# Kernel tuning notes

Hardware: AMD Instinct MI355X
Metric: run time of the kernel (lower is better)

The kernel has to match this reference:

```python
import math
import jax, jax.numpy as jnp
import numpy as np

NEG_INF = -1e9


def maximum_path(neg_cent, text_len, spec_len):
    """Monotonic alignment search (VITS). neg_cent: [B, Ty(spec), Tx(text)].
    Returns hard path [B, Ty, Tx] (float32, 0/1)."""
    B, Ty, Tx = neg_cent.shape
    xs = jnp.arange(Tx)

    # Forward DP over spec frames y; carry = best cumulative value per text pos x.
    def fwd_step(value, inp):
        y, score = inp  # score: [B, Tx]
        diag = jnp.pad(value[:, :-1], ((0, 0), (1, 0)), constant_values=NEG_INF)
        d = diag > value  # move-diagonally indicator for backtracking
        new = score + jnp.maximum(value, diag)
        new = jnp.where(y == 0, jnp.where(xs == 0, score, NEG_INF), new)
        return new, d

    init = jnp.full((B, Tx), NEG_INF, dtype=neg_cent.dtype)
    _, dirs = jax.lax.scan(fwd_step, init,
                           (jnp.arange(Ty), jnp.swapaxes(neg_cent, 0, 1)))
    # dirs: [Ty, B, Tx] bool; dirs[y] compares row y-1 values (as in cython MAS).

    # Backtrack from (spec_len-1, text_len-1) down to y=0.
    def bwd_step(index, inp):
        y, d_row = inp  # index: [B] int32, d_row: [B, Tx]
        active = y < spec_len  # [B]
        row = jnp.where(active[:, None],
                        jax.nn.one_hot(index, Tx, dtype=jnp.float32), 0.0)
        d_at = jnp.take_along_axis(d_row, index[:, None], axis=1)[:, 0]
        move = (index != 0) & ((index == y) | d_at)
        index = jnp.where(active & move, index - 1, index)
        return index, row

    init_idx = text_len - 1
    _, path = jax.lax.scan(bwd_step, init_idx, (jnp.arange(Ty), dirs),
                           reverse=True)
    return jnp.swapaxes(path, 0, 1)  # [B, Ty, Tx]


def setup_inputs() -> dict:
    key = jax.random.key(0)
    ks = jax.random.split(key, 6)
    B, C, Tx, Ty = 8, 192, 512, 2048
    z_p = jax.random.normal(ks[0], (B, C, Ty), dtype=jnp.float32)
    m_p = jax.random.normal(ks[1], (B, C, Tx), dtype=jnp.float32)
    logs_p = 0.1 * jax.random.normal(ks[2], (B, C, Tx), dtype=jnp.float32)
    logs_q = 0.1 * jax.random.normal(ks[3], (B, C, Ty), dtype=jnp.float32)
    text_len = jax.random.randint(ks[4], (B,), Tx * 3 // 4, Tx + 1)
    spec_len = jax.random.randint(ks[5], (B,), Ty * 3 // 4, Ty + 1)
    text_mask = (jnp.arange(Tx)[None, :] < text_len[:, None]).astype(jnp.float32)[:, None, :]
    spec_mask = (jnp.arange(Ty)[None, :] < spec_len[:, None]).astype(jnp.float32)[:, None, :]
    return {"z_p": z_p, "m_p": m_p, "logs_p": logs_p, "logs_q": logs_q,
            "text_mask": text_mask, "spec_mask": spec_mask}


def reference(z_p, m_p, logs_p, logs_q, text_mask, spec_mask):
    text_len = jnp.sum(text_mask, axis=(1, 2)).astype(jnp.int32)  # [B]
    spec_len = jnp.sum(spec_mask, axis=(1, 2)).astype(jnp.int32)  # [B]

    # ---- search_path: neg log-likelihood grid [B, T_spec, T_text] ----
    s_p_sq_r = jnp.exp(-2.0 * logs_p)  # [B, C, Tx]
    nc1 = jnp.sum(-0.5 * math.log(2 * math.pi) - logs_p, axis=1, keepdims=True)  # [B,1,Tx]
    nc2 = jnp.einsum('bct,bcx->btx', -0.5 * z_p * z_p, s_p_sq_r)
    nc3 = jnp.einsum('bct,bcx->btx', z_p, m_p * s_p_sq_r)
    nc4 = jnp.sum(-0.5 * m_p * m_p * s_p_sq_r, axis=1, keepdims=True)  # [B,1,Tx]
    neg_cent = nc1 + nc2 + nc3 + nc4  # [B, Ty, Tx]

    MAS_path = maximum_path(neg_cent, text_len, spec_len)  # [B, Ty, Tx]

    # ---- gather-combine text stats onto spec frames ----
    m_p_a = jnp.einsum('btx,bcx->bct', MAS_path, m_p)      # [B, C, Ty]
    logs_p_a = jnp.einsum('btx,bcx->bct', MAS_path, logs_p)

    # ---- KL divergence loss (VITS) ----
    kl = logs_p_a - logs_q - 0.5 \
        + 0.5 * jnp.square(z_p - m_p_a) * jnp.exp(-2.0 * logs_p_a)
    loss_kl = jnp.sum(kl * spec_mask) / jnp.sum(spec_mask)

    duration = jnp.sum(MAS_path, axis=1)[:, None, :]  # [B, 1, Tx]
    return MAS_path[:, None], m_p_a, logs_p_a, loss_kl, duration
```

## Files before the change

### kernel.cpp

```cpp
#include <hip/hip_runtime.h>
#include <cstdint>
#include <cstddef>

#define BB 8
#define CC 192
#define TXX 512
#define TYY 2048

#define NEG_INF (-1e9f)
#define HALF_LOG_2PI 0.9189385332046727f

#define O1 8388608
#define O2 11534336
#define O3 14680064
#define O4 14680065

#define WS_NEG   0
#define WS_S     33554432
#define WS_MSR   36700160
#define WS_BIAS  39845888
#define WS_DIRS  39862272
#define WS_IDX   40910848
#define WS_LENS  40976384
#define WS_PART  40976448

typedef float f32x4 __attribute__((ext_vector_type(4)));

#define PRE_NZERO 2048
#define PRE_NPREP 3072
#define PRE_NBIAS 16
#define PRE_NLEN  8
__global__ __launch_bounds__(256) void k_pre(const float* __restrict__ logs_p,
                                             const float* __restrict__ m_p,
                                             const float* __restrict__ tmask,
                                             const float* __restrict__ smask,
                                             float* __restrict__ s,
                                             float* __restrict__ msr,
                                             float* __restrict__ bias,
                                             int* __restrict__ lens,
                                             float* __restrict__ out) {
    int blk = blockIdx.x, tid = threadIdx.x;
    if (blk < PRE_NZERO) {
        int64_t i = (int64_t)blk * 256 + tid;
        const int64_t n4 = (int64_t)BB * TYY * TXX / 4;
        float4 z4 = make_float4(0.f, 0.f, 0.f, 0.f);
        float4* p4 = (float4*)out;
        for (int64_t k = i; k < n4; k += (int64_t)PRE_NZERO * 256) p4[k] = z4;
        if (i < BB * TXX) out[O4 + i] = 0.0f;
    } else if (blk < PRE_NZERO + PRE_NPREP) {
        int i = (blk - PRE_NZERO) * 256 + tid;
        float lp = logs_p[i], m = m_p[i];
        float sv = expf(-2.0f * lp);
        s[i] = sv;
        msr[i] = m * sv;
    } else if (blk < PRE_NZERO + PRE_NPREP + PRE_NBIAS) {
        int i = (blk - PRE_NZERO - PRE_NPREP) * 256 + tid;
        int b = i >> 9, x = i & (TXX - 1);
        size_t base = (size_t)b * CC * TXX + x;
        const float* lpb = logs_p + base;
        const float* mb  = m_p + base;
        float acc = 0.f;
#pragma unroll 8
        for (int c = 0; c < CC; ++c) {
            float lp = lpb[(size_t)c * TXX];
            float m  = mb[(size_t)c * TXX];
            float msv = m * expf(-2.0f * lp);
            acc += -HALF_LOG_2PI - lp - 0.5f * m * msv;
        }
        bias[i] = acc;
    } else {
        __shared__ float red[256];
        int b = blk - (PRE_NZERO + PRE_NPREP + PRE_NBIAS);
        float ts = 0.f;
        for (int i = tid; i < TXX; i += 256) ts += tmask[b * TXX + i];
        red[tid] = ts; __syncthreads();
        for (int s2 = 128; s2 > 0; s2 >>= 1) { if (tid < s2) red[tid] += red[tid + s2]; __syncthreads(); }
        if (tid == 0) lens[b] = (int)(red[0] + 0.5f);
        __syncthreads();
        float ss = 0.f;
        for (int i = tid; i < TYY; i += 256) ss += smask[b * TYY + i];
        red[tid] = ss; __syncthreads();
        for (int s2 = 128; s2 > 0; s2 >>= 1) { if (tid < s2) red[tid] += red[tid + s2]; __syncthreads(); }
        if (tid == 0) lens[8 + b] = (int)(red[0] + 0.5f);
    }
}

__global__ __launch_bounds__(256) void k_gemm(const float* __restrict__ z,
                                              const float* __restrict__ msr,
                                              const float* __restrict__ sarr,
                                              const float* __restrict__ bias,
                                              const int* __restrict__ lens,
                                              float* __restrict__ neg) {
    int x0 = blockIdx.x * 64, t0 = blockIdx.y * 64, b = blockIdx.z;
    if (x0 >= lens[b] || t0 >= lens[8 + b]) return;

    __shared__ float Zs[16][68], Ms[16][68], Ss[16][68];
    int tid = threadIdx.x;
    int tx = tid & 15, ty = tid >> 4;
    const float* zb = z    + (size_t)b * CC * TYY;
    const float* mb = msr  + (size_t)b * CC * TXX;
    const float* sb = sarr + (size_t)b * CC * TXX;
    int lr = tid >> 4, lc = (tid & 15) * 4;
    float acc[4][4] = {};
    for (int k0 = 0; k0 < CC; k0 += 16) {
        float4 zv = *(const float4*)(zb + (size_t)(k0 + lr) * TYY + t0 + lc);
        float4 mv = *(const float4*)(mb + (size_t)(k0 + lr) * TXX + x0 + lc);
        float4 sv = *(const float4*)(sb + (size_t)(k0 + lr) * TXX + x0 + lc);
        __syncthreads();
        *(float4*)&Zs[lr][lc] = zv;
        *(float4*)&Ms[lr][lc] = mv;
        *(float4*)&Ss[lr][lc] = sv;
        __syncthreads();
#pragma unroll
        for (int k = 0; k < 16; ++k) {
            float4 a4  = *(const float4*)&Zs[k][ty * 4];
            float4 bm4 = *(const float4*)&Ms[k][tx * 4];
            float4 bs4 = *(const float4*)&Ss[k][tx * 4];
            float av[4]  = {a4.x, a4.y, a4.z, a4.w};
            float bmv[4] = {bm4.x, bm4.y, bm4.z, bm4.w};
            float bsv[4] = {bs4.x, bs4.y, bs4.z, bs4.w};
#pragma unroll
            for (int i2 = 0; i2 < 4; ++i2) {
                float a2 = -0.5f * av[i2] * av[i2];
#pragma unroll
                for (int j = 0; j < 4; ++j)
                    acc[i2][j] += av[i2] * bmv[j] + a2 * bsv[j];
            }
        }
    }
    float4 b4 = *(const float4*)(bias + b * TXX + x0 + tx * 4);
    float bv[4] = {b4.x, b4.y, b4.z, b4.w};
#pragma unroll
    for (int i2 = 0; i2 < 4; ++i2) {
        int t = t0 + ty * 4 + i2;
        float4 o;
        o.x = acc[i2][0] + bv[0]; o.y = acc[i2][1] + bv[1];
        o.z = acc[i2][2] + bv[2]; o.w = acc[i2][3] + bv[3];
        *(float4*)(neg + ((size_t)b * TYY + t) * TXX + x0 + tx * 4) = o;
    }
}

#define GLOAD4(DST, PTR, OFF)                                             \
    asm volatile("global_load_dwordx4 %0, %1, off offset:" #OFF           \
                 : "=v"(DST) : "v"(PTR) : "memory")

#define WAIT_VM(N) do {                                                   \
    asm volatile("s_waitcnt vmcnt(" #N ")" ::: "memory");                 \
    __builtin_amdgcn_sched_barrier(0);                                    \
} while (0)

#define LOADG(DST, G) do {                                                \
    const char* p0_ = (const char*)nc4 + (size_t)(G) * 16384 + lane * 32; \
    const char* p2_ = p0_ + 4096;                                         \
    const char* p4_ = p0_ + 8192;                                         \
    const char* p6_ = p0_ + 12288;                                        \
    GLOAD4(DST[0],  p0_, 0);    GLOAD4(DST[1],  p0_, 16);                 \
    GLOAD4(DST[2],  p0_, 2048); GLOAD4(DST[3],  p0_, 2064);               \
    GLOAD4(DST[4],  p2_, 0);    GLOAD4(DST[5],  p2_, 16);                 \
    GLOAD4(DST[6],  p2_, 2048); GLOAD4(DST[7],  p2_, 2064);               \
    GLOAD4(DST[8],  p4_, 0);    GLOAD4(DST[9],  p4_, 16);                 \
    GLOAD4(DST[10], p4_, 2048); GLOAD4(DST[11], p4_, 2064);               \
    GLOAD4(DST[12], p6_, 0);    GLOAD4(DST[13], p6_, 16);                 \
    GLOAD4(DST[14], p6_, 2048); GLOAD4(DST[15], p6_, 2064);               \
} while (0)

#define DPROW(CUR, YB, R) do {                                                \
    int y_ = (YB) + (R);                                                      \
    float s0_ = CUR[2*(R)][0],   s1_ = CUR[2*(R)][1];                         \
    float s2_ = CUR[2*(R)][2],   s3_ = CUR[2*(R)][3];                         \
    float s4_ = CUR[2*(R)+1][0], s5_ = CUR[2*(R)+1][1];                       \
    float s6_ = CUR[2*(R)+1][2], s7_ = CUR[2*(R)+1][3];                       \
    unsigned d_ = 0;                                                          \
    if (y_ == 0) {                                                            \
        if (lane == 0) v[0] = s0_;             \
    } else {                                                                  \
        float pl_ = __int_as_float(__builtin_amdgcn_update_dpp(               \
            0, __float_as_int(v[7]), 0x138, 0xF, 0xF, false));                \
        if (lane == 0) pl_ = NEG_INF;                                         \
        float n0_ = s0_ + fmaxf(v[0], pl_);  if (pl_  > v[0]) d_ |= 1u;       \
        float n1_ = s1_ + fmaxf(v[1], v[0]); if (v[0] > v[1]) d_ |= 2u;       \
        float n2_ = s2_ + fmaxf(v[2], v[1]); if (v[1] > v[2]) d_ |= 4u;       \
        float n3_ = s3_ + fmaxf(v[3], v[2]); if (v[2] > v[3]) d_ |= 8u;       \
        float n4_ = s4_ + fmaxf(v[4], v[3]); if (v[3] > v[4]) d_ |= 16u;      \
        float n5_ = s5_ + fmaxf(v[5], v[4]); if (v[4] > v[5]) d_ |= 32u;      \
        float n6_ = s6_ + fmaxf(v[6], v[5]); if (v[5] > v[6]) d_ |= 64u;      \
        float n7_ = s7_ + fmaxf(v[7], v[6]); if (v[6] > v[7]) d_ |= 128u;     \
        v[0] = n0_; v[1] = n1_; v[2] = n2_; v[3] = n3_;                       \
        v[4] = n4_; v[5] = n5_; v[6] = n6_; v[7] = n7_;                       \
    }                                                                         \
    unsigned t_ = (unsigned)(y_ - 8 * lane);                                  \
    if (t_ < 8u) d_ |= 1u << t_;                 \
    acc |= d_ << (((R) & 3) * 8);                                             \
    if (((R) & 3) == 3) { db32[(y_ >> 2) * 64 + lane] = acc; acc = 0; }       \
} while (0)

#define FWD_ITER(G, CUR, NXT) do {                                \
    int g_ = (G);                                                 \
    if (g_ + 2 < ng) {                                            \
        LOADG(NXT, g_ + 2);                 \
        WAIT_VM(32);                                              \
    } else if (g_ + 1 < ng) {                                     \
        WAIT_VM(16);                                              \
    } else {                                                      \
        WAIT_VM(0);                                               \
    }                                                             \
    int yb_ = 8 * g_;                                             \
    DPROW(CUR, yb_, 0); DPROW(CUR, yb_, 1);                       \
    DPROW(CUR, yb_, 2); DPROW(CUR, yb_, 3);                       \
    DPROW(CUR, yb_, 4); DPROW(CUR, yb_, 5);                       \
    DPROW(CUR, yb_, 6); DPROW(CUR, yb_, 7);                       \
} while (0)

__global__ __launch_bounds__(64, 1) void k_fwd(const float* __restrict__ neg,
                                               const int* __restrict__ lens,
                                               uint32_t* __restrict__ dirs) {
    int b = blockIdx.x, lane = threadIdx.x;
    const float* nc4 = neg + (size_t)b * TYY * TXX;
    uint32_t* db32 = dirs + (size_t)b * (TYY / 4) * 64;
    int slen = lens[8 + b];
    int ng = (slen + 7) >> 3;

    float v[8];
#pragma unroll
    for (int j = 0; j < 8; ++j) v[j] = NEG_INF;
    unsigned acc = 0;

    f32x4 bufA[16], bufB[16], bufC[16];
    LOADG(bufA, 0);
    LOADG(bufB, 1);

    for (int p = 0; p < ng; p += 3) {
        FWD_ITER(p, bufA, bufC);
        if (p + 1 < ng) FWD_ITER(p + 1, bufB, bufA);
        if (p + 2 < ng) FWD_ITER(p + 2, bufC, bufB);
    }
}

#define LOADW(D0, D1, D2, WB, QROW, BOFF) do {                            \
    const uint32_t* p_ = db32 + (QROW) + 4 * (WB);                        \
    uint32_t a0_=p_[0], a1_=p_[1], a2_=p_[2],  a3_=p_[3];                 \
    uint32_t b0_=p_[4], b1_=p_[5], b2_=p_[6],  b3_=p_[7];                 \
    uint32_t c0_=p_[8], c1_=p_[9], c2_=p_[10], c3_=p_[11];                \
    D0 = ((a0_>>(BOFF))&0xffu)        | (((a1_>>(BOFF))&0xffu)<<8) |      \
         (((a2_>>(BOFF))&0xffu)<<16)  | (((a3_>>(BOFF))&0xffu)<<24);      \
    D1 = ((b0_>>(BOFF))&0xffu)        | (((b1_>>(BOFF))&0xffu)<<8) |      \
         (((b2_>>(BOFF))&0xffu)<<16)  | (((b3_>>(BOFF))&0xffu)<<24);      \
    D2 = ((c0_>>(BOFF))&0xffu)        | (((c1_>>(BOFF))&0xffu)<<8) |      \
         (((c2_>>(BOFF))&0xffu)<<16)  | (((c3_>>(BOFF))&0xffu)<<24);      \
} while (0)

__global__ __launch_bounds__(64, 1) void k_bwd(const int* __restrict__ lens,
                                               const uint32_t* __restrict__ dirs,
                                               int* __restrict__ idx_map,
                                               float* __restrict__ out) {
    int b = blockIdx.x, lane = threadIdx.x;
    const uint32_t* db32 = dirs + (size_t)b * (TYY / 4) * 64;
    int tlen = lens[b], slen = lens[8 + b];

    int idx = tlen - 1;
    int y0 = slen - 1;
    int wb;
    uint32_t W0 = 0, W1 = 0, W2 = 0;
    {
        int yy = y0 - lane; if (yy < 0) yy = 0;
        int qrow = (yy >> 2) * 64, boff = (yy & 3) * 8;
        int t = (idx >> 5) - 1; if (t < 0) t = 0; if (t > 13) t = 13;
        wb = t;
        if (lane < 32) LOADW(W0, W1, W2, wb, qrow, boff);
    }
    while (y0 >= 0) {
        int w0 = (idx >> 5) - 1; if (w0 < 0) w0 = 0; if (w0 > 14) w0 = 14;
        int s = w0 - wb; if (s < 0) s = 0; if (s > 1) s = 1;
        uint32_t lo = s ? W1 : W0;
        uint32_t hi = s ? W2 : W1;
        int base = (wb + s) << 5;
        uint32_t N0 = 0, N1 = 0, N2 = 0;
        int idxm = idx - 32; if (idxm < 0) idxm = 0;
        int wbn = (idxm >> 5) - 1; if (wbn < 0) wbn = 0; if (wbn > 13) wbn = 13;
        {
            int yn = y0 - 32 - lane; if (yn < 0) yn = 0;
            int qn = (yn >> 2) * 64, bn = (yn & 3) * 8;
            if (lane < 32) LOADW(N0, N1, N2, wbn, qn, bn);
        }
        int nsteps = (y0 + 1 < 32) ? y0 + 1 : 32;
        int cap = 0;
#pragma unroll
        for (int j = 0; j < 32; ++j) {
            if (lane == j) cap = idx;
            uint32_t l = (uint32_t)__builtin_amdgcn_readlane((int)lo, j);
            uint32_t h = (uint32_t)__builtin_amdgcn_readlane((int)hi, j);
            int bp = idx - base;
            uint32_t word = (bp & 32) ? h : l;
            idx -= (int)((word >> (bp & 31)) & 1u);
        }
        if (lane < nsteps) {
            int y = y0 - lane;
            idx_map[b * TYY + y] = cap;
            out[((size_t)(b * TYY + y)) * TXX + cap] = 1.0f;
            atomicAdd(&out[O4 + b * TXX + cap], 1.0f);
        }
        wb = wbn; W0 = N0; W1 = N1; W2 = N2;
        y0 -= 32;
    }
}

__global__ __launch_bounds__(256) void k_gather(const float* __restrict__ z_p,
                                                const float* __restrict__ m_p,
                                                const float* __restrict__ logs_p,
                                                const float* __restrict__ logs_q,
                                                const int* __restrict__ lens,
                                                const int* __restrict__ idx_map,
                                                float* __restrict__ out,
                                                float* __restrict__ partials) {
    const int S = BB * CC * TYY / 4;
    int base = blockIdx.x * 256 + threadIdx.x;
    float klsum = 0.f;
#pragma unroll
    for (int r = 0; r < 4; ++r) {
        int i = base + r * S;
        int t = i & (TYY - 1);
        int bc = i >> 11;
        int b = bc / CC;
        float ma = 0.f, la = 0.f;
        if (t < lens[8 + b]) {
            int x = idx_map[b * TYY + t];
            size_t off = (size_t)bc * TXX + x;
            ma = m_p[off];
            la = logs_p[off];
            float zv = z_p[i], lq = logs_q[i];
            float dz = zv - ma;
            klsum += la - lq - 0.5f + 0.5f * dz * dz * expf(-2.0f * la);
        }
        out[O1 + i] = ma;
        out[O2 + i] = la;
    }
    for (int o = 32; o > 0; o >>= 1) klsum += __shfl_down(klsum, o);
    __shared__ float red[4];
    if ((threadIdx.x & 63) == 0) red[threadIdx.x >> 6] = klsum;
    __syncthreads();
    if (threadIdx.x == 0) partials[blockIdx.x] = red[0] + red[1] + red[2] + red[3];
}

__global__ void k_final(const float* __restrict__ partials, const int* __restrict__ lens,
                        float* __restrict__ out) {
    float s = 0.f;
    for (int i = threadIdx.x; i < 3072; i += 256) s += partials[i];
    for (int o = 32; o > 0; o >>= 1) s += __shfl_down(s, o);
    __shared__ float red[4];
    if ((threadIdx.x & 63) == 0) red[threadIdx.x >> 6] = s;
    __syncthreads();
    if (threadIdx.x == 0) {
        float tot = 0.f;
        for (int b = 0; b < 8; ++b) tot += (float)lens[8 + b];
        out[O3] = (red[0] + red[1] + red[2] + red[3]) / tot;
    }
}

extern "C" void kernel_launch(void* const* d_in, const int* in_sizes, int n_in,
                              void* d_out, int out_size, void* d_ws, size_t ws_size,
                              hipStream_t stream) {
    const float* z_p    = (const float*)d_in[0];
    const float* m_p    = (const float*)d_in[1];
    const float* logs_p = (const float*)d_in[2];
    const float* logs_q = (const float*)d_in[3];
    const float* tmask  = (const float*)d_in[4];
    const float* smask  = (const float*)d_in[5];
    float* out = (float*)d_out;
    char* ws = (char*)d_ws;

    float*    neg      = (float*)(ws + WS_NEG);
    float*    sarr     = (float*)(ws + WS_S);
    float*    msr      = (float*)(ws + WS_MSR);
    float*    bias     = (float*)(ws + WS_BIAS);
    uint32_t* dirs     = (uint32_t*)(ws + WS_DIRS);
    int*      idx_map  = (int*)(ws + WS_IDX);
    int*      lens     = (int*)(ws + WS_LENS);
    float*    partials = (float*)(ws + WS_PART);

    hipLaunchKernelGGL(k_pre, dim3(PRE_NZERO + PRE_NPREP + PRE_NBIAS + PRE_NLEN),
                       dim3(256), 0, stream,
                       logs_p, m_p, tmask, smask, sarr, msr, bias, lens, out);
    hipLaunchKernelGGL(k_gemm,   dim3(8, 32, 8), dim3(256), 0, stream,
                       z_p, msr, sarr, bias, lens, neg);
    hipLaunchKernelGGL(k_fwd,    dim3(8),        dim3(64),  0, stream, neg, lens, dirs);
    hipLaunchKernelGGL(k_bwd,    dim3(8),        dim3(64),  0, stream, lens, dirs, idx_map, out);
    hipLaunchKernelGGL(k_gather, dim3(3072),     dim3(256), 0, stream,
                       z_p, m_p, logs_p, logs_q, lens, idx_map, out, partials);
    hipLaunchKernelGGL(k_final,  dim3(1),        dim3(256), 0, stream, partials, lens, out);
}
```

Baseline: 525.4 us.

## Fuse GEMM, forward DP and backtrack into one kernel with per-chunk flag sync

Merges the neg_cent GEMM, the forward DP scan and the backtrack into a single kernel. The first 8 blocks run the per-batch DP and spin on per-(batch, 64-row chunk) atomic counters, which GEMM tile blocks increment with release semantics when their tile is written. The forward scan can therefore start on early rows while later GEMM tiles are still being computed, and two launch boundaries disappear. The risks are spin-wait overhead, DP blocks occupying CUs, and a possible deadlock if the DP blocks run before the GEMM blocks can be scheduled. The counters reuse the partials workspace region and are zeroed by an extra block in k_pre.

```diff
diff --git a/kernel.cpp b/kernel.cpp
--- a/kernel.cpp
+++ b/kernel.cpp
@@ -38,7 +38,8 @@
                                              float* __restrict__ msr,
                                              float* __restrict__ bias,
                                              int* __restrict__ lens,
-                                             float* __restrict__ out) {
+                                             float* __restrict__ out,
+                                             int* __restrict__ cnt) {
     int blk = blockIdx.x, tid = threadIdx.x;
     if (blk < PRE_NZERO) {
         int64_t i = (int64_t)blk * 256 + tid;
@@ -68,7 +69,7 @@
             acc += -HALF_LOG_2PI - lp - 0.5f * m * msv;
         }
         bias[i] = acc;
-    } else {
+    } else if (blk < PRE_NZERO + PRE_NPREP + PRE_NBIAS + PRE_NLEN) {
         __shared__ float red[256];
         int b = blk - (PRE_NZERO + PRE_NPREP + PRE_NBIAS);
         float ts = 0.f;
@@ -82,61 +83,8 @@
         red[tid] = ss; __syncthreads();
         for (int s2 = 128; s2 > 0; s2 >>= 1) { if (tid < s2) red[tid] += red[tid + s2]; __syncthreads(); }
         if (tid == 0) lens[8 + b] = (int)(red[0] + 0.5f);
-    }
-}
-
-__global__ __launch_bounds__(256) void k_gemm(const float* __restrict__ z,
-                                              const float* __restrict__ msr,
-                                              const float* __restrict__ sarr,
-                                              const float* __restrict__ bias,
-                                              const int* __restrict__ lens,
-                                              float* __restrict__ neg) {
-    int x0 = blockIdx.x * 64, t0 = blockIdx.y * 64, b = blockIdx.z;
-    if (x0 >= lens[b] || t0 >= lens[8 + b]) return;
-
-    __shared__ float Zs[16][68], Ms[16][68], Ss[16][68];
-    int tid = threadIdx.x;
-    int tx = tid & 15, ty = tid >> 4;
-    const float* zb = z    + (size_t)b * CC * TYY;
-    const float* mb = msr  + (size_t)b * CC * TXX;
-    const float* sb = sarr + (size_t)b * CC * TXX;
-    int lr = tid >> 4, lc = (tid & 15) * 4;
-    float acc[4][4] = {};
-    for (int k0 = 0; k0 < CC; k0 += 16) {
-        float4 zv = *(const float4*)(zb + (size_t)(k0 + lr) * TYY + t0 + lc);
-        float4 mv = *(const float4*)(mb + (size_t)(k0 + lr) * TXX + x0 + lc);
-        float4 sv = *(const float4*)(sb + (size_t)(k0 + lr) * TXX + x0 + lc);
-        __syncthreads();
-        *(float4*)&Zs[lr][lc] = zv;
-        *(float4*)&Ms[lr][lc] = mv;
-        *(float4*)&Ss[lr][lc] = sv;
-        __syncthreads();
-#pragma unroll
-        for (int k = 0; k < 16; ++k) {
-            float4 a4  = *(const float4*)&Zs[k][ty * 4];
-            float4 bm4 = *(const float4*)&Ms[k][tx * 4];
-            float4 bs4 = *(const float4*)&Ss[k][tx * 4];
-            float av[4]  = {a4.x, a4.y, a4.z, a4.w};
-            float bmv[4] = {bm4.x, bm4.y, bm4.z, bm4.w};
-            float bsv[4] = {bs4.x, bs4.y, bs4.z, bs4.w};
-#pragma unroll
-            for (int i2 = 0; i2 < 4; ++i2) {
-                float a2 = -0.5f * av[i2] * av[i2];
-#pragma unroll
-                for (int j = 0; j < 4; ++j)
-                    acc[i2][j] += av[i2] * bmv[j] + a2 * bsv[j];
-            }
-        }
-    }
-    float4 b4 = *(const float4*)(bias + b * TXX + x0 + tx * 4);
-    float bv[4] = {b4.x, b4.y, b4.z, b4.w};
-#pragma unroll
-    for (int i2 = 0; i2 < 4; ++i2) {
-        int t = t0 + ty * 4 + i2;
-        float4 o;
-        o.x = acc[i2][0] + bv[0]; o.y = acc[i2][1] + bv[1];
-        o.z = acc[i2][2] + bv[2]; o.w = acc[i2][3] + bv[3];
-        *(float4*)(neg + ((size_t)b * TYY + t) * TXX + x0 + tx * 4) = o;
+    } else {
+        cnt[tid] = 0;
     }
 }
 
@@ -194,9 +142,16 @@
     if (((R) & 3) == 3) { db32[(y_ >> 2) * 64 + lane] = acc; acc = 0; }       \
 } while (0)
 
+#define SPIN_CHUNK(C) do {                                                    \
+    while (__hip_atomic_load(&cnt[(b << 5) + (C)], __ATOMIC_ACQUIRE,          \
+                             __HIP_MEMORY_SCOPE_AGENT) < 8)                   \
+        __builtin_amdgcn_s_sleep(2);                                          \
+} while (0)
+
 #define FWD_ITER(G, CUR, NXT) do {                                \
     int g_ = (G);                                                 \
     if (g_ + 2 < ng) {                                            \
+        if (((g_ + 2) & 7) == 0) SPIN_CHUNK((g_ + 2) >> 3);       \
         LOADG(NXT, g_ + 2);                 \
         WAIT_VM(32);                                              \
     } else if (g_ + 1 < ng) {                                     \
@@ -211,31 +166,6 @@
     DPROW(CUR, yb_, 6); DPROW(CUR, yb_, 7);                       \
 } while (0)
 
-__global__ __launch_bounds__(64, 1) void k_fwd(const float* __restrict__ neg,
-                                               const int* __restrict__ lens,
-                                               uint32_t* __restrict__ dirs) {
-    int b = blockIdx.x, lane = threadIdx.x;
-    const float* nc4 = neg + (size_t)b * TYY * TXX;
-    uint32_t* db32 = dirs + (size_t)b * (TYY / 4) * 64;
-    int slen = lens[8 + b];
-    int ng = (slen + 7) >> 3;
-
-    float v[8];
-#pragma unroll
-    for (int j = 0; j < 8; ++j) v[j] = NEG_INF;
-    unsigned acc = 0;
-
-    f32x4 bufA[16], bufB[16], bufC[16];
-    LOADG(bufA, 0);
-    LOADG(bufB, 1);
-
-    for (int p = 0; p < ng; p += 3) {
-        FWD_ITER(p, bufA, bufC);
-        if (p + 1 < ng) FWD_ITER(p + 1, bufB, bufA);
-        if (p + 2 < ng) FWD_ITER(p + 2, bufC, bufB);
-    }
-}
-
 #define LOADW(D0, D1, D2, WB, QROW, BOFF) do {                            \
     const uint32_t* p_ = db32 + (QROW) + 4 * (WB);                        \
     uint32_t a0_=p_[0], a1_=p_[1], a2_=p_[2],  a3_=p_[3];                 \
@@ -249,59 +179,152 @@
          (((c2_>>(BOFF))&0xffu)<<16)  | (((c3_>>(BOFF))&0xffu)<<24);      \
 } while (0)
 
-__global__ __launch_bounds__(64, 1) void k_bwd(const int* __restrict__ lens,
-                                               const uint32_t* __restrict__ dirs,
-                                               int* __restrict__ idx_map,
-                                               float* __restrict__ out) {
-    int b = blockIdx.x, lane = threadIdx.x;
-    const uint32_t* db32 = dirs + (size_t)b * (TYY / 4) * 64;
-    int tlen = lens[b], slen = lens[8 + b];
-
-    int idx = tlen - 1;
-    int y0 = slen - 1;
-    int wb;
-    uint32_t W0 = 0, W1 = 0, W2 = 0;
-    {
-        int yy = y0 - lane; if (yy < 0) yy = 0;
-        int qrow = (yy >> 2) * 64, boff = (yy & 3) * 8;
-        int t = (idx >> 5) - 1; if (t < 0) t = 0; if (t > 13) t = 13;
-        wb = t;
-        if (lane < 32) LOADW(W0, W1, W2, wb, qrow, boff);
+__global__ __launch_bounds__(256) void k_mega(const float* __restrict__ z,
+                                              const float* __restrict__ msr,
+                                              const float* __restrict__ sarr,
+                                              const float* __restrict__ bias,
+                                              const int* __restrict__ lens,
+                                              float* __restrict__ neg,
+                                              uint32_t* __restrict__ dirs,
+                                              int* __restrict__ idx_map,
+                                              float* __restrict__ out,
+                                              int* __restrict__ cnt) {
+    __shared__ float Zs[16][68], Ms[16][68], Ss[16][68];
+    int id = blockIdx.x;
+
+    if (id < 8) {
+        if (threadIdx.x >= 64) return;
+        int b = id, lane = threadIdx.x;
+        const float* nc4 = neg + (size_t)b * TYY * TXX;
+        uint32_t* db32 = dirs + (size_t)b * (TYY / 4) * 64;
+        int slen = lens[8 + b];
+        int ng = (slen + 7) >> 3;
+
+        float v[8];
+#pragma unroll
+        for (int j = 0; j < 8; ++j) v[j] = NEG_INF;
+        unsigned acc = 0;
+
+        f32x4 bufA[16], bufB[16], bufC[16];
+        SPIN_CHUNK(0);
+        LOADG(bufA, 0);
+        LOADG(bufB, 1);
+
+        for (int p = 0; p < ng; p += 3) {
+            FWD_ITER(p, bufA, bufC);
+            if (p + 1 < ng) FWD_ITER(p + 1, bufB, bufA);
+            if (p + 2 < ng) FWD_ITER(p + 2, bufC, bufB);
+        }
+
+        WAIT_VM(0);
+        {
+            int tlen = lens[b];
+            int idx = tlen - 1;
+            int y0 = slen - 1;
+            int wb;
+            uint32_t W0 = 0, W1 = 0, W2 = 0;
+            {
+                int yy = y0 - lane; if (yy < 0) yy = 0;
+                int qrow = (yy >> 2) * 64, boff = (yy & 3) * 8;
+                int t = (idx >> 5) - 1; if (t < 0) t = 0; if (t > 13) t = 13;
+                wb = t;
+                if (lane < 32) LOADW(W0, W1, W2, wb, qrow, boff);
+            }
+            while (y0 >= 0) {
+                int w0 = (idx >> 5) - 1; if (w0 < 0) w0 = 0; if (w0 > 14) w0 = 14;
+                int s = w0 - wb; if (s < 0) s = 0; if (s > 1) s = 1;
+                uint32_t lo = s ? W1 : W0;
+                uint32_t hi = s ? W2 : W1;
+                int base = (wb + s) << 5;
+                uint32_t N0 = 0, N1 = 0, N2 = 0;
+                int idxm = idx - 32; if (idxm < 0) idxm = 0;
+                int wbn = (idxm >> 5) - 1; if (wbn < 0) wbn = 0; if (wbn > 13) wbn = 13;
+                {
+                    int yn = y0 - 32 - lane; if (yn < 0) yn = 0;
+                    int qn = (yn >> 2) * 64, bn = (yn & 3) * 8;
+                    if (lane < 32) LOADW(N0, N1, N2, wbn, qn, bn);
+                }
+                int nsteps = (y0 + 1 < 32) ? y0 + 1 : 32;
+                int cap = 0;
+#pragma unroll
+                for (int j = 0; j < 32; ++j) {
+                    if (lane == j) cap = idx;
+                    uint32_t l = (uint32_t)__builtin_amdgcn_readlane((int)lo, j);
+                    uint32_t h = (uint32_t)__builtin_amdgcn_readlane((int)hi, j);
+                    int bp = idx - base;
+                    uint32_t word = (bp & 32) ? h : l;
+                    idx -= (int)((word >> (bp & 31)) & 1u);
+                }
+                if (lane < nsteps) {
+                    int y = y0 - lane;
+                    idx_map[b * TYY + y] = cap;
+                    out[((size_t)(b * TYY + y)) * TXX + cap] = 1.0f;
+                    atomicAdd(&out[O4 + b * TXX + cap], 1.0f);
+                }
+                wb = wbn; W0 = N0; W1 = N1; W2 = N2;
+                y0 -= 32;
+            }
+        }
+        return;
     }
-    while (y0 >= 0) {
-        int w0 = (idx >> 5) - 1; if (w0 < 0) w0 = 0; if (w0 > 14) w0 = 14;
-        int s = w0 - wb; if (s < 0) s = 0; if (s > 1) s = 1;
-        uint32_t lo = s ? W1 : W0;
-        uint32_t hi = s ? W2 : W1;
-        int base = (wb + s) << 5;
-        uint32_t N0 = 0, N1 = 0, N2 = 0;
-        int idxm = idx - 32; if (idxm < 0) idxm = 0;
-        int wbn = (idxm >> 5) - 1; if (wbn < 0) wbn = 0; if (wbn > 13) wbn = 13;
-        {
-            int yn = y0 - 32 - lane; if (yn < 0) yn = 0;
-            int qn = (yn >> 2) * 64, bn = (yn & 3) * 8;
-            if (lane < 32) LOADW(N0, N1, N2, wbn, qn, bn);
-        }
-        int nsteps = (y0 + 1 < 32) ? y0 + 1 : 32;
-        int cap = 0;
-#pragma unroll
-        for (int j = 0; j < 32; ++j) {
-            if (lane == j) cap = idx;
-            uint32_t l = (uint32_t)__builtin_amdgcn_readlane((int)lo, j);
-            uint32_t h = (uint32_t)__builtin_amdgcn_readlane((int)hi, j);
-            int bp = idx - base;
-            uint32_t word = (bp & 32) ? h : l;
-            idx -= (int)((word >> (bp & 31)) & 1u);
-        }
-        if (lane < nsteps) {
-            int y = y0 - lane;
-            idx_map[b * TYY + y] = cap;
-            out[((size_t)(b * TYY + y)) * TXX + cap] = 1.0f;
-            atomicAdd(&out[O4 + b * TXX + cap], 1.0f);
-        }
-        wb = wbn; W0 = N0; W1 = N1; W2 = N2;
-        y0 -= 32;
+
+    int gid = id - 8;
+    int tch = gid >> 6;
+    int rem = gid & 63;
+    int b   = rem >> 3;
+    int x0  = (rem & 7) * 64;
+    int t0  = tch * 64;
+    int tid = threadIdx.x;
+    bool live = (x0 < lens[b] && t0 < lens[8 + b]);
+    if (live) {
+        int tx = tid & 15, ty = tid >> 4;
+        const float* zb = z    + (size_t)b * CC * TYY;
+        const float* mb = msr  + (size_t)b * CC * TXX;
+        const float* sb = sarr + (size_t)b * CC * TXX;
+        int lr = tid >> 4, lc = (tid & 15) * 4;
+        float gacc[4][4] = {};
+        for (int k0 = 0; k0 < CC; k0 += 16) {
+            float4 zv = *(const float4*)(zb + (size_t)(k0 + lr) * TYY + t0 + lc);
+            float4 mv = *(const float4*)(mb + (size_t)(k0 + lr) * TXX + x0 + lc);
+            float4 sv = *(const float4*)(sb + (size_t)(k0 + lr) * TXX + x0 + lc);
+            __syncthreads();
+            *(float4*)&Zs[lr][lc] = zv;
+            *(float4*)&Ms[lr][lc] = mv;
+            *(float4*)&Ss[lr][lc] = sv;
+            __syncthreads();
+#pragma unroll
+            for (int k = 0; k < 16; ++k) {
+                float4 a4  = *(const float4*)&Zs[k][ty * 4];
+                float4 bm4 = *(const float4*)&Ms[k][tx * 4];
+                float4 bs4 = *(const float4*)&Ss[k][tx * 4];
+                float av[4]  = {a4.x, a4.y, a4.z, a4.w};
+                float bmv[4] = {bm4.x, bm4.y, bm4.z, bm4.w};
+                float bsv[4] = {bs4.x, bs4.y, bs4.z, bs4.w};
+#pragma unroll
+                for (int i2 = 0; i2 < 4; ++i2) {
+                    float a2 = -0.5f * av[i2] * av[i2];
+#pragma unroll
+                    for (int j = 0; j < 4; ++j)
+                        gacc[i2][j] += av[i2] * bmv[j] + a2 * bsv[j];
+                }
+            }
+        }
+        float4 b4 = *(const float4*)(bias + b * TXX + x0 + tx * 4);
+        float bv[4] = {b4.x, b4.y, b4.z, b4.w};
+#pragma unroll
+        for (int i2 = 0; i2 < 4; ++i2) {
+            int t = t0 + ty * 4 + i2;
+            float4 o;
+            o.x = gacc[i2][0] + bv[0]; o.y = gacc[i2][1] + bv[1];
+            o.z = gacc[i2][2] + bv[2]; o.w = gacc[i2][3] + bv[3];
+            *(float4*)(neg + ((size_t)b * TYY + t) * TXX + x0 + tx * 4) = o;
+        }
     }
+    __threadfence();
+    __syncthreads();
+    if (tid == 0)
+        __hip_atomic_fetch_add(&cnt[(b << 5) + tch], 1,
+                               __ATOMIC_RELEASE, __HIP_MEMORY_SCOPE_AGENT);
 }
 
 __global__ __launch_bounds__(256) void k_gather(const float* __restrict__ z_p,
@@ -376,14 +399,14 @@
     int*      idx_map  = (int*)(ws + WS_IDX);
     int*      lens     = (int*)(ws + WS_LENS);
     float*    partials = (float*)(ws + WS_PART);
-
-    hipLaunchKernelGGL(k_pre, dim3(PRE_NZERO + PRE_NPREP + PRE_NBIAS + PRE_NLEN),
+    int*      cnt      = (int*)(ws + WS_PART);
+
+    hipLaunchKernelGGL(k_pre,
+                       dim3(PRE_NZERO + PRE_NPREP + PRE_NBIAS + PRE_NLEN + 1),
                        dim3(256), 0, stream,
-                       logs_p, m_p, tmask, smask, sarr, msr, bias, lens, out);
-    hipLaunchKernelGGL(k_gemm,   dim3(8, 32, 8), dim3(256), 0, stream,
-                       z_p, msr, sarr, bias, lens, neg);
-    hipLaunchKernelGGL(k_fwd,    dim3(8),        dim3(64),  0, stream, neg, lens, dirs);
-    hipLaunchKernelGGL(k_bwd,    dim3(8),        dim3(64),  0, stream, lens, dirs, idx_map, out);
+                       logs_p, m_p, tmask, smask, sarr, msr, bias, lens, out, cnt);
+    hipLaunchKernelGGL(k_mega,   dim3(2056),     dim3(256), 0, stream,
+                       z_p, msr, sarr, bias, lens, neg, dirs, idx_map, out, cnt);
     hipLaunchKernelGGL(k_gather, dim3(3072),     dim3(256), 0, stream,
                        z_p, m_p, logs_p, logs_q, lens, idx_map, out, partials);
     hipLaunchKernelGGL(k_final,  dim3(1),        dim3(256), 0, stream, partials, lens, out);
```

Result: slower. 649.4 us (+23.6%).

## Fuse output zeroing into GEMM launch and prefetch backtrack direction words asynchronously

Applied to the files above, without the earlier changes.

Moves the zero-fill of the large output path tensor out of the preprocessing kernel and into the GEMM launch as extra blocks, so the memory-bound zeroing runs alongside the compute-bound GEMM tiles. In the serial backtrack kernel, the next chunk's direction words are now fetched with raw inline-asm loads issued before the 32-step readlane loop. The wait and byte-packing happen after the loop, so global load latency overlaps with the dependent backtrack chain. This relies on explicit waitcnt and scheduling barriers, and reduces the number of zeroing blocks.

```diff
diff --git a/kernel.cpp b/kernel.cpp
--- a/kernel.cpp
+++ b/kernel.cpp
@@ -26,7 +26,6 @@
 
 typedef float f32x4 __attribute__((ext_vector_type(4)));
 
-#define PRE_NZERO 2048
 #define PRE_NPREP 3072
 #define PRE_NBIAS 16
 #define PRE_NLEN  8
@@ -37,24 +36,16 @@
                                              float* __restrict__ s,
                                              float* __restrict__ msr,
                                              float* __restrict__ bias,
-                                             int* __restrict__ lens,
-                                             float* __restrict__ out) {
+                                             int* __restrict__ lens) {
     int blk = blockIdx.x, tid = threadIdx.x;
-    if (blk < PRE_NZERO) {
-        int64_t i = (int64_t)blk * 256 + tid;
-        const int64_t n4 = (int64_t)BB * TYY * TXX / 4;
-        float4 z4 = make_float4(0.f, 0.f, 0.f, 0.f);
-        float4* p4 = (float4*)out;
-        for (int64_t k = i; k < n4; k += (int64_t)PRE_NZERO * 256) p4[k] = z4;
-        if (i < BB * TXX) out[O4 + i] = 0.0f;
-    } else if (blk < PRE_NZERO + PRE_NPREP) {
-        int i = (blk - PRE_NZERO) * 256 + tid;
+    if (blk < PRE_NPREP) {
+        int i = blk * 256 + tid;
         float lp = logs_p[i], m = m_p[i];
         float sv = expf(-2.0f * lp);
         s[i] = sv;
         msr[i] = m * sv;
-    } else if (blk < PRE_NZERO + PRE_NPREP + PRE_NBIAS) {
-        int i = (blk - PRE_NZERO - PRE_NPREP) * 256 + tid;
+    } else if (blk < PRE_NPREP + PRE_NBIAS) {
+        int i = (blk - PRE_NPREP) * 256 + tid;
         int b = i >> 9, x = i & (TXX - 1);
         size_t base = (size_t)b * CC * TXX + x;
         const float* lpb = logs_p + base;
@@ -70,7 +61,7 @@
         bias[i] = acc;
     } else {
         __shared__ float red[256];
-        int b = blk - (PRE_NZERO + PRE_NPREP + PRE_NBIAS);
+        int b = blk - (PRE_NPREP + PRE_NBIAS);
         float ts = 0.f;
         for (int i = tid; i < TXX; i += 256) ts += tmask[b * TXX + i];
         red[tid] = ts; __syncthreads();
@@ -85,17 +76,29 @@
     }
 }
 
-__global__ __launch_bounds__(256) void k_gemm(const float* __restrict__ z,
-                                              const float* __restrict__ msr,
-                                              const float* __restrict__ sarr,
-                                              const float* __restrict__ bias,
-                                              const int* __restrict__ lens,
-                                              float* __restrict__ neg) {
-    int x0 = blockIdx.x * 64, t0 = blockIdx.y * 64, b = blockIdx.z;
+#define GZ_NZERO 512
+__global__ __launch_bounds__(256) void k_gz(const float* __restrict__ z,
+                                            const float* __restrict__ msr,
+                                            const float* __restrict__ sarr,
+                                            const float* __restrict__ bias,
+                                            const int* __restrict__ lens,
+                                            float* __restrict__ neg,
+                                            float* __restrict__ out) {
+    int id = blockIdx.x, tid = threadIdx.x;
+    if (id < GZ_NZERO) {
+        int64_t i = (int64_t)id * 256 + tid;
+        const int64_t n4 = (int64_t)BB * TYY * TXX / 4;
+        float4 z4 = make_float4(0.f, 0.f, 0.f, 0.f);
+        float4* p4 = (float4*)out;
+        for (int64_t k = i; k < n4; k += (int64_t)GZ_NZERO * 256) p4[k] = z4;
+        if (i < BB * TXX) out[O4 + i] = 0.0f;
+        return;
+    }
+    int gid = id - GZ_NZERO;
+    int x0 = (gid & 7) * 64, t0 = ((gid >> 3) & 31) * 64, b = gid >> 8;
     if (x0 >= lens[b] || t0 >= lens[8 + b]) return;
 
     __shared__ float Zs[16][68], Ms[16][68], Ss[16][68];
-    int tid = threadIdx.x;
     int tx = tid & 15, ty = tid >> 4;
     const float* zb = z    + (size_t)b * CC * TYY;
     const float* mb = msr  + (size_t)b * CC * TXX;
@@ -142,6 +145,10 @@
 
 #define GLOAD4(DST, PTR, OFF)                                             \
     asm volatile("global_load_dwordx4 %0, %1, off offset:" #OFF           \
+                 : "=v"(DST) : "v"(PTR) : "memory")
+
+#define GLOADD(DST, PTR)                                                  \
+    asm volatile("global_load_dword %0, %1, off"                          \
                  : "=v"(DST) : "v"(PTR) : "memory")
 
 #define WAIT_VM(N) do {                                                   \
@@ -236,17 +243,23 @@
     }
 }
 
-#define LOADW(D0, D1, D2, WB, QROW, BOFF) do {                            \
+#define RAWLD(NR, WB, QROW) do {                                          \
     const uint32_t* p_ = db32 + (QROW) + 4 * (WB);                        \
-    uint32_t a0_=p_[0], a1_=p_[1], a2_=p_[2],  a3_=p_[3];                 \
-    uint32_t b0_=p_[4], b1_=p_[5], b2_=p_[6],  b3_=p_[7];                 \
-    uint32_t c0_=p_[8], c1_=p_[9], c2_=p_[10], c3_=p_[11];                \
-    D0 = ((a0_>>(BOFF))&0xffu)        | (((a1_>>(BOFF))&0xffu)<<8) |      \
-         (((a2_>>(BOFF))&0xffu)<<16)  | (((a3_>>(BOFF))&0xffu)<<24);      \
-    D1 = ((b0_>>(BOFF))&0xffu)        | (((b1_>>(BOFF))&0xffu)<<8) |      \
-         (((b2_>>(BOFF))&0xffu)<<16)  | (((b3_>>(BOFF))&0xffu)<<24);      \
-    D2 = ((c0_>>(BOFF))&0xffu)        | (((c1_>>(BOFF))&0xffu)<<8) |      \
-         (((c2_>>(BOFF))&0xffu)<<16)  | (((c3_>>(BOFF))&0xffu)<<24);      \
+    GLOADD(NR[0],  (p_ + 0));  GLOADD(NR[1],  (p_ + 1));                  \
+    GLOADD(NR[2],  (p_ + 2));  GLOADD(NR[3],  (p_ + 3));                  \
+    GLOADD(NR[4],  (p_ + 4));  GLOADD(NR[5],  (p_ + 5));                  \
+    GLOADD(NR[6],  (p_ + 6));  GLOADD(NR[7],  (p_ + 7));                  \
+    GLOADD(NR[8],  (p_ + 8));  GLOADD(NR[9],  (p_ + 9));                  \
+    GLOADD(NR[10], (p_ + 10)); GLOADD(NR[11], (p_ + 11));                 \
+} while (0)
+
+#define PACKW(W0, W1, W2, NR, BOFF) do {                                  \
+    W0 = ((NR[0]>>(BOFF))&0xffu)        | (((NR[1]>>(BOFF))&0xffu)<<8) |  \
+         (((NR[2]>>(BOFF))&0xffu)<<16)  | (((NR[3]>>(BOFF))&0xffu)<<24);  \
+    W1 = ((NR[4]>>(BOFF))&0xffu)        | (((NR[5]>>(BOFF))&0xffu)<<8) |  \
+         (((NR[6]>>(BOFF))&0xffu)<<16)  | (((NR[7]>>(BOFF))&0xffu)<<24);  \
+    W2 = ((NR[8]>>(BOFF))&0xffu)        | (((NR[9]>>(BOFF))&0xffu)<<8) |  \
+         (((NR[10]>>(BOFF))&0xffu)<<16) | (((NR[11]>>(BOFF))&0xffu)<<24); \
 } while (0)
 
 __global__ __launch_bounds__(64, 1) void k_bwd(const int* __restrict__ lens,
@@ -266,7 +279,13 @@
         int qrow = (yy >> 2) * 64, boff = (yy & 3) * 8;
         int t = (idx >> 5) - 1; if (t < 0) t = 0; if (t > 13) t = 13;
         wb = t;
-        if (lane < 32) LOADW(W0, W1, W2, wb, qrow, boff);
+        uint32_t R[12];
+        if (lane < 32) {
+            RAWLD(R, wb, qrow);
+            asm volatile("s_waitcnt vmcnt(0)" ::: "memory");
+            __builtin_amdgcn_sched_barrier(0);
+            PACKW(W0, W1, W2, R, boff);
+        }
     }
     while (y0 >= 0) {
         int w0 = (idx >> 5) - 1; if (w0 < 0) w0 = 0; if (w0 > 14) w0 = 14;
@@ -274,14 +293,13 @@
         uint32_t lo = s ? W1 : W0;
         uint32_t hi = s ? W2 : W1;
         int base = (wb + s) << 5;
-        uint32_t N0 = 0, N1 = 0, N2 = 0;
+        uint32_t N[12];
         int idxm = idx - 32; if (idxm < 0) idxm = 0;
         int wbn = (idxm >> 5) - 1; if (wbn < 0) wbn = 0; if (wbn > 13) wbn = 13;
-        {
-            int yn = y0 - 32 - lane; if (yn < 0) yn = 0;
-            int qn = (yn >> 2) * 64, bn = (yn & 3) * 8;
-            if (lane < 32) LOADW(N0, N1, N2, wbn, qn, bn);
-        }
+        int yn = y0 - 32 - lane; if (yn < 0) yn = 0;
+        int qn = (yn >> 2) * 64, bn = (yn & 3) * 8;
+        if (lane < 32) RAWLD(N, wbn, qn);
+        __builtin_amdgcn_sched_barrier(0);
         int nsteps = (y0 + 1 < 32) ? y0 + 1 : 32;
         int cap = 0;
 #pragma unroll
@@ -293,13 +311,17 @@
             uint32_t word = (bp & 32) ? h : l;
             idx -= (int)((word >> (bp & 31)) & 1u);
         }
+        __builtin_amdgcn_sched_barrier(0);
+        asm volatile("s_waitcnt vmcnt(0)" ::: "memory");
+        __builtin_amdgcn_sched_barrier(0);
+        PACKW(W0, W1, W2, N, bn);
+        wb = wbn;
         if (lane < nsteps) {
             int y = y0 - lane;
             idx_map[b * TYY + y] = cap;
             out[((size_t)(b * TYY + y)) * TXX + cap] = 1.0f;
             atomicAdd(&out[O4 + b * TXX + cap], 1.0f);
         }
-        wb = wbn; W0 = N0; W1 = N1; W2 = N2;
         y0 -= 32;
     }
 }
@@ -377,11 +399,11 @@
     int*      lens     = (int*)(ws + WS_LENS);
     float*    partials = (float*)(ws + WS_PART);
 
-    hipLaunchKernelGGL(k_pre, dim3(PRE_NZERO + PRE_NPREP + PRE_NBIAS + PRE_NLEN),
+    hipLaunchKernelGGL(k_pre,    dim3(PRE_NPREP + PRE_NBIAS + PRE_NLEN),
                        dim3(256), 0, stream,
-                       logs_p, m_p, tmask, smask, sarr, msr, bias, lens, out);
-    hipLaunchKernelGGL(k_gemm,   dim3(8, 32, 8), dim3(256), 0, stream,
-                       z_p, msr, sarr, bias, lens, neg);
+                       logs_p, m_p, tmask, smask, sarr, msr, bias, lens);
+    hipLaunchKernelGGL(k_gz,     dim3(GZ_NZERO + 2048), dim3(256), 0, stream,
+                       z_p, msr, sarr, bias, lens, neg, out);
     hipLaunchKernelGGL(k_fwd,    dim3(8),        dim3(64),  0, stream, neg, lens, dirs);
     hipLaunchKernelGGL(k_bwd,    dim3(8),        dim3(64),  0, stream, lens, dirs, idx_map, out);
     hipLaunchKernelGGL(k_gather, dim3(3072),     dim3(256), 0, stream,
```

After: 500.5 us. 4.7% less time.
